# Kernel optimization log

Hardware: AMD Instinct MI355X
Metric: run time of the kernel (lower is better)

Reference implementation:

```python
import jax, jax.numpy as jnp
import numpy as np

B, N, F_IN, F_HID, OUT_DIM = 16, 64, 128, 256, 768
C_IN = 2                      # adjs channels after cat([A, 1-A])
H_T = max(C_IN, OUT_DIM) * 2  # 1536, translate_mlp hidden
D_T = C_IN + 2 * OUT_DIM      # 1538, translate_mlp input
D_R = C_IN + OUT_DIM          # 770, final_read_score input
H_R = 2 * D_R                 # 1540, final_read_score hidden
BN_EPS = 1e-5


def mask_x(x, flags):
    # x: [B,N,F], flags: [B,N]
    return x * flags[:, :, None]


def mask_adjs(adjs, flags):
    # adjs: [B,C,N,N]
    return adjs * (flags[:, None, :, None] * flags[:, None, None, :])


def batchnorm_train(h, gamma, beta):
    # BatchNorm1d in training mode over flattened batch dim (biased var)
    mu = jnp.mean(h, axis=0)
    var = jnp.mean(jnp.square(h - mu), axis=0)
    return gamma * (h - mu) * jax.lax.rsqrt(var + BN_EPS) + beta


def setup_inputs() -> dict:
    key = jax.random.key(0)
    ks = jax.random.split(key, 12)
    def w(k, shape, fan_in):
        return jax.random.normal(k, shape, jnp.float32) / np.float32(np.sqrt(fan_in))
    return {
        "x": jax.random.normal(ks[0], (B, N, F_IN), jnp.float32),
        "adjs": jax.random.uniform(ks[1], (B, N, N), dtype=jnp.float32),
        "node_flags": jnp.ones((B, N), jnp.float32),
        # GIN: multi-channel graph conv (2 channels) + output projection
        "Wg": w(ks[2], (C_IN * F_IN, F_HID), C_IN * F_IN),
        "bg": jnp.zeros((F_HID,), jnp.float32),
        "Wout": w(ks[3], (F_IN + F_HID, OUT_DIM), F_IN + F_HID),
        "bout": jnp.zeros((OUT_DIM,), jnp.float32),
        # translate_mlp: 2-layer MLP with BN, elu
        "W1t": w(ks[4], (D_T, H_T), D_T),
        "b1t": jnp.zeros((H_T,), jnp.float32),
        "gamma_t": jnp.ones((H_T,), jnp.float32),
        "beta_t": jnp.zeros((H_T,), jnp.float32),
        "W2t": w(ks[5], (H_T, OUT_DIM), H_T),
        "b2t": jnp.zeros((OUT_DIM,), jnp.float32),
        # final_read_score: 2-layer MLP, no BN
        "W1r": w(ks[6], (D_R, H_R), D_R),
        "b1r": jnp.zeros((H_R,), jnp.float32),
        "W2r": w(ks[7], (H_R, 1), H_R),
        "b2r": jnp.zeros((1,), jnp.float32),
    }


def reference(x, adjs, node_flags, Wg, bg, Wout, bout,
              W1t, b1t, gamma_t, beta_t, W2t, b2t,
              W1r, b1r, W2r, b2r):
    # ---- build 2-channel adjacency [B,2,N,N] and mask ----
    A = jnp.stack([adjs, 1.0 - adjs], axis=1)
    A = mask_adjs(A, node_flags)

    # ---- GIN (2-channel message passing, dropout=identity / eval) ----
    # per-channel aggregation A_c @ x, concat channels -> [B,N,2*F_IN]
    h = jnp.einsum('bcij,bjf->bicf', A, x).reshape(B, N, C_IN * F_IN)
    h = jax.nn.elu(h @ Wg + bg)
    h = mask_x(h, node_flags)
    x_o = jnp.tanh(jnp.concatenate([x, h], axis=-1) @ Wout + bout)
    x_o = mask_x(x_o, node_flags)  # [B,N,768]

    # ---- node_feature_to_matrix: pairwise features [B,N,N,2*768] ----
    xp = jnp.concatenate([
        jnp.broadcast_to(x_o[:, :, None, :], (B, N, N, OUT_DIM)),
        jnp.broadcast_to(x_o[:, None, :, :], (B, N, N, OUT_DIM)),
    ], axis=-1)
    mlp_in = jnp.concatenate([jnp.transpose(A, (0, 2, 3, 1)), xp], axis=-1)  # [B,N,N,1538]

    # ---- translate_mlp per edge (BN training-mode stats over B*N*N) ----
    flat = mlp_in.reshape(-1, D_T)
    hmid = jax.nn.elu(batchnorm_train(flat @ W1t + b1t, gamma_t, beta_t))
    new_adjs = (hmid @ W2t + b2t).reshape(B, N, N, OUT_DIM).transpose(0, 3, 1, 2)
    new_adjs = new_adjs + jnp.swapaxes(new_adjs, -1, -2)  # symmetrize
    new_adjs = mask_adjs(new_adjs, node_flags)            # [B,768,N,N]

    # ---- final_read_score over stacked channels [B,770,N,N] ----
    stacked = jnp.concatenate([A, new_adjs], axis=1)
    r_in = jnp.transpose(stacked, (0, 2, 3, 1))           # [B,N,N,770]
    hr = jax.nn.elu(r_in @ W1r + b1r)
    score = (hr @ W2r + b2r)[..., 0]                      # [B,N,N]

    mask = 1.0 - jnp.eye(N, dtype=score.dtype)            # zero diagonal
    return (score * mask[None], x_o)
```

## Files before the change

kernel.cpp:

```cpp
#include <hip/hip_runtime.h>
#include <cstdint>
#include <cstddef>

#define NQPAD 1664
#define KC 192
#define NPAIR 2016
#define PROW 2048

typedef __bf16 bf16x8 __attribute__((ext_vector_type(8)));
typedef float  f32x4  __attribute__((ext_vector_type(4)));
typedef unsigned short ushort_t;

__device__ __forceinline__ unsigned short f2bf(float f) {
  union { float f; unsigned u; } v; v.f = f;
  unsigned r = v.u + 0x7fffu + ((v.u >> 16) & 1u);
  return (unsigned short)(r >> 16);
}
__device__ __forceinline__ float bf2f(unsigned short h) {
  union { unsigned u; float f; } v; v.u = ((unsigned)h) << 16;
  return v.f;
}
__device__ __forceinline__ float elu_f(float x) {
  return x > 0.f ? x : __expf(x) - 1.f;
}

__device__ __forceinline__ void cp16_lds(const ushort_t* g, ushort_t* l) {
  __builtin_amdgcn_global_load_lds(
      (const __attribute__((address_space(1))) void*)g,
      (__attribute__((address_space(3))) void*)l, 16, 0, 0);
}

__global__ void k_zero(float* p, int n) {
  int i = blockIdx.x * blockDim.x + threadIdx.x;
  if (i < n) p[i] = 0.f;
}

__global__ void k_diag(float* out) {
  int t = blockIdx.x * 256 + threadIdx.x;
  int b = t >> 6, i = t & 63;
  out[((size_t)b * 64 + i) * 64 + i] = 0.f;
}

__global__ void k_agg(const float* __restrict__ x, const float* __restrict__ adjs,
                      const float* __restrict__ flags,
                      float* __restrict__ h0, float* __restrict__ concat) {
  const int bi = blockIdx.x;
  const int b = bi >> 6, i = bi & 63;
  const int f = threadIdx.x;
  __shared__ float sa[64], sm[64];
  if (f < 64) {
    float m = flags[b * 64 + i] * flags[b * 64 + f];
    float a = adjs[(size_t)(b * 64 + i) * 64 + f] * m;
    sa[f] = a; sm[f] = m;
  }
  __syncthreads();
  float s0 = 0.f, s1 = 0.f;
  const float* xb = x + (size_t)b * 64 * 128;
  for (int j = 0; j < 64; ++j) {
    float xv = xb[j * 128 + f];
    s0 = fmaf(sa[j], xv, s0);
    s1 = fmaf(sm[j] - sa[j], xv, s1);
  }
  h0[(size_t)bi * 256 + f]       = s0;
  h0[(size_t)bi * 256 + 128 + f] = s1;
  concat[(size_t)bi * 384 + f]   = xb[i * 128 + f];
}

__global__ __launch_bounds__(256) void k_sgemm(
    const float* __restrict__ A, const float* __restrict__ Bm,
    float* __restrict__ Cf, ushort_t* __restrict__ Cb,
    const float* __restrict__ bias, const float* __restrict__ rowscale,
    int K, int lda, int ldb, int ldc, int act) {
  __shared__ float As[64 * 17];
  __shared__ float Bs[16 * 64];
  const int tid = threadIdx.x;
  const int tx = tid & 15, ty = tid >> 4;
  const int m0 = blockIdx.y * 64, n0 = blockIdx.x * 64;
  float acc[4][4] = {};
  for (int k0 = 0; k0 < K; k0 += 16) {
#pragma unroll
    for (int i = 0; i < 4; i++) {
      int e = tid + i * 256;
      int r = e >> 4, c = e & 15;
      As[r * 17 + c] = A[(size_t)(m0 + r) * lda + k0 + c];
      int rb = e >> 6, cb = e & 63;
      Bs[e] = Bm[(size_t)(k0 + rb) * ldb + n0 + cb];
    }
    __syncthreads();
#pragma unroll
    for (int kk = 0; kk < 16; kk++) {
      float av[4], bv[4];
#pragma unroll
      for (int i = 0; i < 4; i++) av[i] = As[(ty * 4 + i) * 17 + kk];
#pragma unroll
      for (int j = 0; j < 4; j++) bv[j] = Bs[kk * 64 + tx * 4 + j];
#pragma unroll
      for (int i = 0; i < 4; i++)
#pragma unroll
        for (int j = 0; j < 4; j++) acc[i][j] = fmaf(av[i], bv[j], acc[i][j]);
    }
    __syncthreads();
  }
#pragma unroll
  for (int i = 0; i < 4; i++) {
    const int mm = m0 + ty * 4 + i;
    const float rs = rowscale ? rowscale[mm] : 1.f;
#pragma unroll
    for (int j = 0; j < 4; j++) {
      const int nn = n0 + tx * 4 + j;
      float v = acc[i][j] + (bias ? bias[nn] : 0.f);
      if (act == 1) v = elu_f(v);
      else if (act == 2) v = tanhf(v);
      v *= rs;
      if (Cf) Cf[(size_t)mm * ldc + nn] = v;
      if (Cb) Cb[(size_t)mm * ldc + nn] = f2bf(v);
    }
  }
}

__global__ void k_castT(const float* __restrict__ in, ushort_t* __restrict__ out,
                        int R, int C, int Cpad, int r0, int ld) {
  __shared__ float t[32][33];
  const int rb = blockIdx.y * 32, cb = blockIdx.x * 32;
  const int tx = threadIdx.x, ty = threadIdx.y;
#pragma unroll
  for (int dy = 0; dy < 32; dy += 8) {
    int r = rb + ty + dy, c = cb + tx;
    t[ty + dy][tx] = (r < R && c < C) ? in[(size_t)(r0 + r) * ld + c] : 0.f;
  }
  __syncthreads();
#pragma unroll
  for (int dy = 0; dy < 32; dy += 8) {
    int c = cb + ty + dy, r = rb + tx;
    if (c < Cpad && r < R) out[(size_t)c * R + r] = f2bf(t[tx][ty + dy]);
  }
}

__global__ void k_cast(const float* __restrict__ in, ushort_t* __restrict__ out, int n) {
  int i = blockIdx.x * blockDim.x + threadIdx.x;
  if (i < n) out[i] = f2bf(in[i]);
}

__global__ __launch_bounds__(256) void k_gemm(
    const ushort_t* __restrict__ A, const ushort_t* __restrict__ BT,
    float* __restrict__ outF, ushort_t* __restrict__ outB,
    int K, int lda, int ldb, int ldc, int ncap, int tiledB) {
  __shared__ __align__(16) ushort_t As[128 * 32];
  __shared__ __align__(16) ushort_t Bs[128 * 32];
  const int tid = threadIdx.x;
  const int lane = tid & 63;
  const int wv = tid >> 6;
  const int m0 = blockIdx.y * 128;
  const int n0 = blockIdx.x * 128;
  const int wm = wv >> 1, wn = wv & 1;

  f32x4 z4 = {0.f, 0.f, 0.f, 0.f};
  f32x4 acc[4][4];
#pragma unroll
  for (int i = 0; i < 4; i++)
#pragma unroll
    for (int j = 0; j < 4; j++) acc[i][j] = z4;

  const int srow = lane & 15;
  const int schunk = lane >> 4;
  const ushort_t* gA0 = A + (size_t)(m0 + 2 * wv * 16 + srow) * lda + schunk * 8;
  const ushort_t* gA1 = gA0 + (size_t)16 * lda;
  const ushort_t* gB0 = BT + (size_t)(n0 + 2 * wv * 16 + srow) * ldb + schunk * 8;
  const ushort_t* gB1 = gB0 + (size_t)16 * ldb;
  ushort_t* lA0 = &As[(2 * wv) * 512];
  ushort_t* lA1 = &As[(2 * wv + 1) * 512];
  ushort_t* lB0 = &Bs[(2 * wv) * 512];
  ushort_t* lB1 = &Bs[(2 * wv + 1) * 512];

  for (int k0 = 0; k0 < K; k0 += 32) {
    cp16_lds(gA0 + k0, lA0);
    cp16_lds(gA1 + k0, lA1);
    cp16_lds(gB0 + k0, lB0);
    cp16_lds(gB1 + k0, lB1);
    __syncthreads();
    bf16x8 af[4], bfv[4];
#pragma unroll
    for (int f = 0; f < 4; ++f) {
      af[f]  = *reinterpret_cast<const bf16x8*>(&As[(wm * 4 + f) * 512 + lane * 8]);
      bfv[f] = *reinterpret_cast<const bf16x8*>(&Bs[(wn * 4 + f) * 512 + lane * 8]);
    }
#pragma unroll
    for (int fm = 0; fm < 4; ++fm)
#pragma unroll
      for (int fn = 0; fn < 4; ++fn)
        acc[fm][fn] = __builtin_amdgcn_mfma_f32_16x16x32_bf16(af[fm], bfv[fn], acc[fm][fn], 0, 0, 0);
    __syncthreads();
  }

  const int er = (lane >> 4) * 4;
  const int ec = lane & 15;
#pragma unroll
  for (int fm = 0; fm < 4; ++fm) {
#pragma unroll
    for (int fn = 0; fn < 4; ++fn) {
      const int nn = n0 + wn * 64 + fn * 16 + ec;
      if (nn >= ncap) continue;
#pragma unroll
      for (int r = 0; r < 4; ++r) {
        const int mm = m0 + wm * 64 + fm * 16 + er + r;
        float v = acc[fm][fn][r];
        if (outF) outF[(size_t)mm * ldc + nn] = v;
        if (outB) {
          if (tiledB)
            outB[((size_t)(mm >> 4) * KC + (nn >> 3)) * 128 + (mm & 15) * 8 + (nn & 7)] = f2bf(v);
          else
            outB[(size_t)mm * ldc + nn] = f2bf(v);
        }
      }
    }
  }
}

__global__ __launch_bounds__(256) void k_gemm_t(
    const ushort_t* __restrict__ At, const ushort_t* __restrict__ Bt,
    ushort_t* __restrict__ outB, int ldc, int ncap, int swz) {
  __shared__ __align__(16) ushort_t As[128 * 32];
  __shared__ __align__(16) ushort_t Bs[128 * 32];
  const int tid = threadIdx.x;
  const int lane = tid & 63;
  const int wv = tid >> 6;

  int bx = blockIdx.x, by = blockIdx.y;
  if (swz && (gridDim.y & 7) == 0) {
    int nb = gridDim.x;
    int linear = bx + nb * by;
    int xcd = linear & 7;
    int slot = linear >> 3;
    int mper = gridDim.y >> 3;
    int mp = slot / nb;
    int n  = slot - mp * nb;
    bx = n; by = xcd * mper + mp;
  }
  const int m0 = by * 128;
  const int n0 = bx * 128;
  const int wm = wv >> 1, wn = wv & 1;

  f32x4 z4 = {0.f, 0.f, 0.f, 0.f};
  f32x4 acc[4][4];
#pragma unroll
  for (int i = 0; i < 4; i++)
#pragma unroll
    for (int j = 0; j < 4; j++) acc[i][j] = z4;

  const ushort_t* gA0 = At + ((size_t)(by * 8 + 2 * wv) * KC) * 128 + lane * 8;
  const ushort_t* gA1 = gA0 + (size_t)KC * 128;
  const ushort_t* gB0 = Bt + ((size_t)(bx * 8 + 2 * wv) * KC) * 128 + lane * 8;
  const ushort_t* gB1 = gB0 + (size_t)KC * 128;
  ushort_t* lA0 = &As[(2 * wv) * 512];
  ushort_t* lA1 = &As[(2 * wv + 1) * 512];
  ushort_t* lB0 = &Bs[(2 * wv) * 512];
  ushort_t* lB1 = &Bs[(2 * wv + 1) * 512];

  for (int c0 = 0; c0 < KC; c0 += 4) {
    const size_t go = (size_t)c0 * 128;
    cp16_lds(gA0 + go, lA0);
    cp16_lds(gA1 + go, lA1);
    cp16_lds(gB0 + go, lB0);
    cp16_lds(gB1 + go, lB1);
    __syncthreads();
    bf16x8 af[4], bfv[4];
#pragma unroll
    for (int f = 0; f < 4; ++f) {
      af[f]  = *reinterpret_cast<const bf16x8*>(&As[(wm * 4 + f) * 512 + lane * 8]);
      bfv[f] = *reinterpret_cast<const bf16x8*>(&Bs[(wn * 4 + f) * 512 + lane * 8]);
    }
#pragma unroll
    for (int fm = 0; fm < 4; ++fm)
#pragma unroll
      for (int fn = 0; fn < 4; ++fn)
        acc[fm][fn] = __builtin_amdgcn_mfma_f32_16x16x32_bf16(af[fm], bfv[fn], acc[fm][fn], 0, 0, 0);
    __syncthreads();
  }

  const int er = (lane >> 4) * 4;
  const int ec = lane & 15;
#pragma unroll
  for (int fm = 0; fm < 4; ++fm) {
#pragma unroll
    for (int fn = 0; fn < 4; ++fn) {
      const int nn = n0 + wn * 64 + fn * 16 + ec;
      if (nn >= ncap) continue;
#pragma unroll
      for (int r = 0; r < 4; ++r) {
        const int mm = m0 + wm * 64 + fm * 16 + er + r;
        outB[(size_t)mm * ldc + nn] = f2bf(acc[fm][fn][r]);
      }
    }
  }
}

__global__ void k_pdat(const float* __restrict__ adjs, const float* __restrict__ flags,
                       float4* __restrict__ pdat) {
  const int b = blockIdx.x;
  const int p = blockIdx.y * 256 + threadIdx.x;
  float4 v;
  if (p < NPAIR) {
    int i = (int)((127.f - sqrtf(16129.f - 8.f * (float)p)) * 0.5f);
    if (i < 0) i = 0;
    while (63 * (i + 1) - (((i + 1) * i) >> 1) <= p) ++i;
    while (63 * i - ((i * (i - 1)) >> 1) > p) --i;
    int j = p - (63 * i - ((i * (i - 1)) >> 1)) + i + 1;
    float m = flags[b * 64 + i] * flags[b * 64 + j];
    float a0ij = adjs[((size_t)b * 64 + i) * 64 + j] * m;
    float a0ji = adjs[((size_t)b * 64 + j) * 64 + i] * m;
    v = make_float4(a0ij, a0ji, m, __int_as_float(i * 64 + j));
  } else {
    v = make_float4(0.f, 0.f, 0.f, __int_as_float(-1));
  }
  pdat[(size_t)b * PROW + p] = v;
}

__global__ __launch_bounds__(256) void k_score2(
    const ushort_t* __restrict__ q, const float4* __restrict__ pdat,
    const float* __restrict__ W1r, const float* __restrict__ b1r,
    const float* __restrict__ W2r, const float* __restrict__ dvec2,
    const float* __restrict__ b2r, float* __restrict__ out, int b0) {
  const int p = blockIdx.x;
  const int bl = blockIdx.y;
  const int b = b0 + bl;
  const int t = threadIdx.x;
  float4 pd = pdat[(size_t)b * PROW + p];
  const int ij = __float_as_int(pd.w);
  const int i = ij >> 6, j = ij & 63;
  const float m = pd.z;
  const float a0ij = pd.x, a1ij = m - pd.x;
  const float a0ji = pd.y, a1ji = m - pd.y;
  const ushort_t* qp = q + ((size_t)bl * PROW + p) * NQPAD;
  float s1 = 0.f, s2 = 0.f;
  for (int n = t; n < 1540; n += 256) {
    float quv = bf2f(qp[n]) + dvec2[n];
    float base = fmaf(m, quv, b1r[n]);
    float w0 = W1r[n], w1 = W1r[1540 + n], w2 = W2r[n];
    float z1 = base + a0ij * w0 + a1ij * w1;
    float z2 = base + a0ji * w0 + a1ji * w1;
    s1 = fmaf(elu_f(z1), w2, s1);
    s2 = fmaf(elu_f(z2), w2, s2);
  }
  __shared__ float red[512];
  red[t] = s1; red[256 + t] = s2;
  __syncthreads();
  for (int s = 128; s > 0; s >>= 1) {
    if (t < s) { red[t] += red[t + s]; red[256 + t] += red[256 + t + s]; }
    __syncthreads();
  }
  if (t == 0) {
    out[((size_t)b * 64 + i) * 64 + j] = red[0]   + b2r[0];
    out[((size_t)b * 64 + j) * 64 + i] = red[256] + b2r[0];
  }
}

__global__ void k_dvec(const float* __restrict__ b2t, const float* __restrict__ W1r,
                       float* __restrict__ dvec2) {
  int n = blockIdx.x * 256 + threadIdx.x;
  if (n >= 1540) return;
  int m0 = blockIdx.y * 96;
  float s = 0.f;
  for (int m2 = m0; m2 < m0 + 96; ++m2)
    s = fmaf(b2t[m2], W1r[(size_t)(2 + m2) * 1540 + n], s);
  atomicAdd(&dvec2[n], 2.f * s);
}

__global__ __launch_bounds__(64) void k_adjsum(
    const float* __restrict__ adjs, const float* __restrict__ flags,
    float* __restrict__ r0s, float* __restrict__ r1s,
    float* __restrict__ c0s, float* __restrict__ c1s, float* __restrict__ scal) {
  const int b = blockIdx.x, t = threadIdx.x;
  __shared__ float f[64];
  __shared__ float red[192];
  f[t] = flags[b * 64 + t];
  __syncthreads();
  const float ft = f[t];
  float r0 = 0, r1 = 0, q0 = 0, q1 = 0, pp = 0;
  for (int j = 0; j < 64; ++j) {
    float m = ft * f[j];
    float a = adjs[((size_t)b * 64 + t) * 64 + j] * m;
    float a1 = m - a;
    r0 += a; r1 += a1;
    q0 = fmaf(a, a, q0); q1 = fmaf(a1, a1, q1); pp = fmaf(a, a1, pp);
  }
  r0s[b * 64 + t] = r0; r1s[b * 64 + t] = r1;
  float c0 = 0, c1 = 0;
  for (int i = 0; i < 64; ++i) {
    float m = f[i] * ft;
    float a = adjs[((size_t)b * 64 + i) * 64 + t] * m;
    c0 += a; c1 += m - a;
  }
  c0s[b * 64 + t] = c0; c1s[b * 64 + t] = c1;
  red[t] = r0; red[64 + t] = r1; red[128 + t] = q0;
  __syncthreads();
  for (int s = 32; s > 0; s >>= 1) {
    if (t < s) { red[t] += red[t + s]; red[64 + t] += red[64 + t + s]; red[128 + t] += red[128 + t + s]; }
    __syncthreads();
  }
  if (t == 0) { scal[b * 5 + 0] = red[0]; scal[b * 5 + 1] = red[64]; scal[b * 5 + 2] = red[128]; }
  __syncthreads();
  red[t] = q1; red[64 + t] = pp;
  __syncthreads();
  for (int s = 32; s > 0; s >>= 1) {
    if (t < s) { red[t] += red[t + s]; red[64 + t] += red[64 + t + s]; }
    __syncthreads();
  }
  if (t == 0) { scal[b * 5 + 3] = red[0]; scal[b * 5 + 4] = red[64]; }
}

__global__ __launch_bounds__(256) void k_stats2(
    const float* __restrict__ UV, const float* __restrict__ W1t,
    const float* __restrict__ b1t,
    const float* __restrict__ r0s, const float* __restrict__ r1s,
    const float* __restrict__ c0s, const float* __restrict__ c1s,
    const float* __restrict__ scal,
    float* __restrict__ colsum, float* __restrict__ colss) {
  const int b = blockIdx.x;
  const int n = blockIdx.y * 256 + threadIdx.x;
  const int t = threadIdx.x;
  __shared__ float sr0[64], sr1[64], sc0[64], sc1[64];
  if (t < 64) {
    sr0[t] = r0s[b * 64 + t]; sr1[t] = r1s[b * 64 + t];
    sc0[t] = c0s[b * 64 + t]; sc1[t] = c1s[b * 64 + t];
  }
  __syncthreads();
  const float S0 = scal[b * 5], S1 = scal[b * 5 + 1], Q0 = scal[b * 5 + 2],
              Q1 = scal[b * 5 + 3], P = scal[b * 5 + 4];
  const float w0 = W1t[n], w1 = W1t[1536 + n], beta = b1t[n];
  float eU = 0, eV = 0, qU = 0, qV = 0, ur0 = 0, ur1 = 0, vc0 = 0, vc1 = 0;
  const float* base = UV + (size_t)b * 64 * 3072;
  for (int idx = 0; idx < 64; ++idx) {
    float U = base[(size_t)idx * 3072 + n];
    float V = base[(size_t)idx * 3072 + 1536 + n];
    eU += U; eV += V;
    qU = fmaf(U, U, qU); qV = fmaf(V, V, qV);
    ur0 = fmaf(U, sr0[idx], ur0); ur1 = fmaf(U, sr1[idx], ur1);
    vc0 = fmaf(V, sc0[idx], vc0); vc1 = fmaf(V, sc1[idx], vc1);
  }
  float hsum = 64.f * (eU + eV) + S0 * w0 + S1 * w1 + 4096.f * beta;
  float hss = 64.f * (qU + qV) + Q0 * w0 * w0 + Q1 * w1 * w1 + 4096.f * beta * beta
    + 2.f * (eU * eV + w0 * ur0 + w1 * ur1 + w0 * vc0 + w1 * vc1
             + 64.f * beta * (eU + eV) + w0 * w1 * P + beta * (w0 * S0 + w1 * S1));
  atomicAdd(&colsum[n], hsum);
  atomicAdd(&colss[n], hss);
}

__global__ void k_bnfin(const float* __restrict__ colsum, const float* __restrict__ colss,
                        const float* __restrict__ gamma, const float* __restrict__ beta,
                        float* __restrict__ bns, float* __restrict__ bnt) {
  int n = blockIdx.x * 256 + threadIdx.x;
  if (n >= 1536) return;
  float mu = colsum[n] * (1.f / 65536.f);
  float var = colss[n] * (1.f / 65536.f) - mu * mu;
  float s = gamma[n] * rsqrtf(var + 1e-5f);
  bns[n] = s;
  bnt[n] = beta[n] - mu * s;
}

__global__ __launch_bounds__(256) void k_act4(
    const float* __restrict__ UV, const float4* __restrict__ pdat,
    const float* __restrict__ W1t, const float* __restrict__ b1t,
    const float* __restrict__ bns, const float* __restrict__ bnt,
    ushort_t* __restrict__ hmid_s, int b0) {
  const int g = blockIdx.x;
  const int b = b0 + (g >> 7);
  const int p0 = (g & 127) * 16;
  const int t = threadIdx.x;
  __shared__ __align__(16) ushort_t tile[KC * 128];
  float w06[6], w16[6], s6[6], t6[6], bb6[6];
#pragma unroll
  for (int c = 0; c < 6; c++) {
    int n = t + 256 * c;
    w06[c] = W1t[n]; w16[c] = W1t[1536 + n];
    s6[c] = bns[n]; t6[c] = bnt[n]; bb6[c] = b1t[n];
  }
  const unsigned short zbf = 0;
  for (int ei = 0; ei < 16; ++ei) {
    const int p = p0 + ei;
    float4 pd = pdat[(size_t)b * PROW + p];
    int ij = __float_as_int(pd.w);
    if (ij >= 0) {
      int i = ij >> 6, j = ij & 63;
      const float* Ui = UV + (size_t)(b * 64 + i) * 3072;
      const float* Vi = Ui + 1536;
      const float* Uj = UV + (size_t)(b * 64 + j) * 3072;
      const float* Vj = Uj + 1536;
      float m = pd.z;
      float a0ij = pd.x, a1ij = m - pd.x;
      float a0ji = pd.y, a1ji = m - pd.y;
#pragma unroll
      for (int c = 0; c < 6; c++) {
        int n = t + 256 * c;
        float h1 = Ui[n] + Vj[n] + a0ij * w06[c] + a1ij * w16[c] + bb6[c];
        float h2 = Uj[n] + Vi[n] + a0ji * w06[c] + a1ji * w16[c] + bb6[c];
        float v = elu_f(fmaf(h1, s6[c], t6[c])) + elu_f(fmaf(h2, s6[c], t6[c]));
        int cc = n >> 3;
        int s = (ei + cc) & 15;
        tile[cc * 128 + s * 8 + (n & 7)] = f2bf(v);
      }
    } else {
#pragma unroll
      for (int c = 0; c < 6; c++) {
        int n = t + 256 * c;
        int cc = n >> 3;
        int s = (ei + cc) & 15;
        tile[cc * 128 + s * 8 + (n & 7)] = zbf;
      }
    }
  }
  __syncthreads();
  uint4* gout = (uint4*)(hmid_s + (size_t)g * (KC * 128));
  const uint4* lt = (const uint4*)tile;
#pragma unroll
  for (int it = 0; it < 12; ++it) {
    int u = t + 256 * it;
    int cc = u >> 4, r = u & 15;
    gout[u] = lt[cc * 16 + ((r + cc) & 15)];
  }
}

extern "C" void kernel_launch(void* const* d_in, const int* in_sizes, int n_in,
                              void* d_out, int out_size, void* d_ws, size_t ws_size,
                              hipStream_t stream) {
  const float* x     = (const float*)d_in[0];
  const float* adjs  = (const float*)d_in[1];
  const float* flags = (const float*)d_in[2];
  const float* Wg    = (const float*)d_in[3];
  const float* bg    = (const float*)d_in[4];
  const float* Wout  = (const float*)d_in[5];
  const float* bout  = (const float*)d_in[6];
  const float* W1t   = (const float*)d_in[7];
  const float* b1t   = (const float*)d_in[8];
  const float* gamma = (const float*)d_in[9];
  const float* beta  = (const float*)d_in[10];
  const float* W2t   = (const float*)d_in[11];
  const float* b2t   = (const float*)d_in[12];
  const float* W1r   = (const float*)d_in[13];
  const float* b1r   = (const float*)d_in[14];
  const float* W2r   = (const float*)d_in[15];
  const float* b2r   = (const float*)d_in[16];
  float* out_score = (float*)d_out;
  float* out_xo    = (float*)d_out + 65536;

  uint8_t* ws = (uint8_t*)d_ws;
  size_t off = 0;
  auto alloc = [&](size_t bytes) -> void* {
    void* p = ws + off;
    off += (bytes + 255) & ~(size_t)255;
    return p;
  };
  float*    h0      = (float*)   alloc((size_t)1024 * 256 * 4);
  float*    concat  = (float*)   alloc((size_t)1024 * 384 * 4);
  ushort_t* xo_bf   = (ushort_t*)alloc((size_t)1024 * 768 * 2);
  ushort_t* W1tT    = (ushort_t*)alloc((size_t)3072 * 768 * 2);
  ushort_t* W2t_bf  = (ushort_t*)alloc((size_t)1536 * 768 * 2);
  ushort_t* WrxT    = (ushort_t*)alloc((size_t)NQPAD * 768 * 2);
  ushort_t* WcT     = (ushort_t*)alloc((size_t)NQPAD * 1536 * 2);
  float*    UV      = (float*)   alloc((size_t)1024 * 3072 * 4);
  float*    dvec2   = (float*)   alloc((size_t)1664 * 4);
  float*    colsum  = (float*)   alloc((size_t)1536 * 4);
  float*    colss   = (float*)   alloc((size_t)1536 * 4);
  float*    bns     = (float*)   alloc((size_t)1536 * 4);
  float*    bnt     = (float*)   alloc((size_t)1536 * 4);
  float*    r0s     = (float*)   alloc((size_t)1024 * 4);
  float*    r1s     = (float*)   alloc((size_t)1024 * 4);
  float*    c0s     = (float*)   alloc((size_t)1024 * 4);
  float*    c1s     = (float*)   alloc((size_t)1024 * 4);
  float*    scal    = (float*)   alloc((size_t)80 * 4);
  float4*   pdat    = (float4*)  alloc((size_t)16 * PROW * 16);

  int cb = 2;
  {
    const int cands[4] = {16, 8, 4, 2};
    for (int ci = 0; ci < 4; ++ci) {
      int c = cands[ci];
      size_t need = off + ((size_t)c * PROW * 1536 * 2 + 256)
                        + ((size_t)c * PROW * NQPAD * 2 + 256);
      if (need <= ws_size) { cb = c; break; }
    }
  }
  ushort_t* hmid_s  = (ushort_t*)alloc((size_t)cb * PROW * 1536 * 2);
  ushort_t* q_c     = (ushort_t*)alloc((size_t)cb * PROW * NQPAD * 2);
  (void)in_sizes; (void)n_in; (void)out_size;

  k_zero<<<dim3(19), dim3(256), 0, stream>>>(dvec2, 1664 + 1536 + 1536);
  k_diag<<<dim3(4), dim3(256), 0, stream>>>(out_score);

  k_agg<<<dim3(1024), dim3(128), 0, stream>>>(x, adjs, flags, h0, concat);
  k_sgemm<<<dim3(4, 16), dim3(256), 0, stream>>>(h0, Wg, concat + 128, (ushort_t*)nullptr,
                                                 bg, flags, 256, 256, 256, 384, 1);
  k_sgemm<<<dim3(12, 16), dim3(256), 0, stream>>>(concat, Wout, out_xo, xo_bf,
                                                  bout, flags, 384, 384, 768, 768, 2);

  k_castT<<<dim3(48, 24), dim3(32, 8), 0, stream>>>(W1t, W1tT, 768, 1536, 1536, 2, 1536);
  k_castT<<<dim3(48, 24), dim3(32, 8), 0, stream>>>(W1t, W1tT + (size_t)1536 * 768, 768, 1536, 1536, 770, 1536);
  k_castT<<<dim3(52, 24), dim3(32, 8), 0, stream>>>(W1r, WrxT, 768, 1540, NQPAD, 2, 1540);
  k_cast<<<dim3(4608), dim3(256), 0, stream>>>(W2t, W2t_bf, 1536 * 768);
  k_adjsum<<<dim3(16), dim3(64), 0, stream>>>(adjs, flags, r0s, r1s, c0s, c1s, scal);
  k_pdat<<<dim3(16, 8), dim3(256), 0, stream>>>(adjs, flags, pdat);

  k_gemm<<<dim3(24, 8), dim3(256), 0, stream>>>(xo_bf, W1tT, UV, (ushort_t*)nullptr,
                                                768, 768, 768, 3072, 3072, 0);
  k_gemm<<<dim3(12, 13), dim3(256), 0, stream>>>(WrxT, W2t_bf, (float*)nullptr, WcT,
                                                 768, 768, 768, 1536, 1536, 1);
  k_dvec<<<dim3(7, 8), dim3(256), 0, stream>>>(b2t, W1r, dvec2);

  k_stats2<<<dim3(16, 6), dim3(256), 0, stream>>>(UV, W1t, b1t, r0s, r1s, c0s, c1s, scal,
                                                  colsum, colss);
  k_bnfin<<<dim3(6), dim3(256), 0, stream>>>(colsum, colss, gamma, beta, bns, bnt);

  for (int b0 = 0; b0 < 16; b0 += cb) {
    k_act4<<<dim3(cb * 128), dim3(256), 0, stream>>>(UV, pdat, W1t, b1t, bns, bnt,
                                                     hmid_s, b0);
    k_gemm_t<<<dim3(13, cb * 16), dim3(256), 0, stream>>>(hmid_s, WcT, q_c,
                                                          NQPAD, 1540, 1);
    k_score2<<<dim3(NPAIR, cb), dim3(256), 0, stream>>>(q_c, pdat, W1r, b1r, W2r,
                                                        dvec2, b2r, out_score, b0);
  }
}
```

Measured before the change: 538.9 us.

## Merge prep kernels, vectorize score reduction, narrow q stride, restructure act loop

Merges the zero and diagonal-clear kernels into one launch, and the three transposed casts plus the W2t cast into one 3D-grid launch, cutting launch count. Narrows the q buffer row stride from 1664 to 1544 to shrink the intermediate's memory traffic. k_score2 now reads 8 bf16 values per thread in one vector load and reduces with wave shuffles instead of a shared-memory tree. k_act4 swaps its loop order so each column's weights are loaded once and the row-i U/V values are reused across consecutive pairs with the same i. The q stride must stay consistent with what the GEMM writes; a 1544-element row is 16-byte aligned, so the uint4 load should be valid.

```diff
diff --git a/kernel.cpp b/kernel.cpp
--- a/kernel.cpp
+++ b/kernel.cpp
@@ -3,6 +3,7 @@
 #include <cstddef>
 
 #define NQPAD 1664
+#define QLD 1544
 #define KC 192
 #define NPAIR 2016
 #define PROW 2048
@@ -30,15 +31,13 @@
       (__attribute__((address_space(3))) void*)l, 16, 0, 0);
 }
 
-__global__ void k_zero(float* p, int n) {
-  int i = blockIdx.x * blockDim.x + threadIdx.x;
-  if (i < n) p[i] = 0.f;
-}
-
-__global__ void k_diag(float* out) {
-  int t = blockIdx.x * 256 + threadIdx.x;
-  int b = t >> 6, i = t & 63;
-  out[((size_t)b * 64 + i) * 64 + i] = 0.f;
+__global__ void k_prep(float* acc, int nacc, float* out) {
+  int id = blockIdx.x * 256 + threadIdx.x;
+  if (id < nacc) acc[id] = 0.f;
+  if (id < 1024) {
+    int b = id >> 6, i = id & 63;
+    out[((size_t)b * 64 + i) * 64 + i] = 0.f;
+  }
 }
 
 __global__ void k_agg(const float* __restrict__ x, const float* __restrict__ adjs,
@@ -118,10 +117,11 @@
   }
 }
 
-__global__ void k_castT(const float* __restrict__ in, ushort_t* __restrict__ out,
-                        int R, int C, int Cpad, int r0, int ld) {
+__device__ __forceinline__ void castT_body(const float* in, ushort_t* out,
+                                           int R, int C, int Cpad, int r0, int ld,
+                                           int bx, int by) {
   __shared__ float t[32][33];
-  const int rb = blockIdx.y * 32, cb = blockIdx.x * 32;
+  const int rb = by * 32, cb = bx * 32;
   const int tx = threadIdx.x, ty = threadIdx.y;
 #pragma unroll
   for (int dy = 0; dy < 32; dy += 8) {
@@ -136,9 +136,22 @@
   }
 }
 
-__global__ void k_cast(const float* __restrict__ in, ushort_t* __restrict__ out, int n) {
-  int i = blockIdx.x * blockDim.x + threadIdx.x;
-  if (i < n) out[i] = f2bf(in[i]);
+__global__ void k_wprep(const float* __restrict__ W1t, const float* __restrict__ W1r,
+                        const float* __restrict__ W2t,
+                        ushort_t* __restrict__ W1tT, ushort_t* __restrict__ WrxT,
+                        ushort_t* __restrict__ W2t_bf) {
+  const int z = blockIdx.z;
+  if (z == 0) {
+    if (blockIdx.x < 48) castT_body(W1t, W1tT, 768, 1536, 1536, 2, 1536, blockIdx.x, blockIdx.y);
+  } else if (z == 1) {
+    if (blockIdx.x < 48) castT_body(W1t, W1tT + (size_t)1536 * 768, 768, 1536, 1536, 770, 1536, blockIdx.x, blockIdx.y);
+  } else if (z == 2) {
+    castT_body(W1r, WrxT, 768, 1540, NQPAD, 2, 1540, blockIdx.x, blockIdx.y);
+  } else {
+    int id = (blockIdx.y * 52 + blockIdx.x) * 256 + threadIdx.y * 32 + threadIdx.x;
+    for (int e = id; e < 1536 * 768; e += 52 * 24 * 256)
+      W2t_bf[e] = f2bf(W2t[e]);
+  }
 }
 
 __global__ __launch_bounds__(256) void k_gemm(
@@ -330,27 +343,36 @@
   const float m = pd.z;
   const float a0ij = pd.x, a1ij = m - pd.x;
   const float a0ji = pd.y, a1ji = m - pd.y;
-  const ushort_t* qp = q + ((size_t)bl * PROW + p) * NQPAD;
   float s1 = 0.f, s2 = 0.f;
-  for (int n = t; n < 1540; n += 256) {
-    float quv = bf2f(qp[n]) + dvec2[n];
-    float base = fmaf(m, quv, b1r[n]);
-    float w0 = W1r[n], w1 = W1r[1540 + n], w2 = W2r[n];
-    float z1 = base + a0ij * w0 + a1ij * w1;
-    float z2 = base + a0ji * w0 + a1ji * w1;
-    s1 = fmaf(elu_f(z1), w2, s1);
-    s2 = fmaf(elu_f(z2), w2, s2);
-  }
-  __shared__ float red[512];
-  red[t] = s1; red[256 + t] = s2;
-  __syncthreads();
-  for (int s = 128; s > 0; s >>= 1) {
-    if (t < s) { red[t] += red[t + s]; red[256 + t] += red[256 + t + s]; }
-    __syncthreads();
-  }
+  const int n0 = t * 8;
+  if (n0 < 1540) {
+    const ushort_t* qp = q + ((size_t)bl * PROW + p) * QLD + n0;
+    uint4 qv = *(const uint4*)qp;
+#pragma unroll
+    for (int k = 0; k < 8; ++k) {
+      int n = n0 + k;
+      if (n < 1540) {
+        float quv = bf2f(((const ushort_t*)&qv)[k]) + dvec2[n];
+        float base = fmaf(m, quv, b1r[n]);
+        float w0 = W1r[n], w1 = W1r[1540 + n], w2 = W2r[n];
+        float z1 = base + a0ij * w0 + a1ij * w1;
+        float z2 = base + a0ji * w0 + a1ji * w1;
+        s1 = fmaf(elu_f(z1), w2, s1);
+        s2 = fmaf(elu_f(z2), w2, s2);
+      }
+    }
+  }
+#pragma unroll
+  for (int mask = 1; mask < 64; mask <<= 1) {
+    s1 += __shfl_xor(s1, mask, 64);
+    s2 += __shfl_xor(s2, mask, 64);
+  }
+  __shared__ float r1[4], r2[4];
+  if ((t & 63) == 0) { r1[t >> 6] = s1; r2[t >> 6] = s2; }
+  __syncthreads();
   if (t == 0) {
-    out[((size_t)b * 64 + i) * 64 + j] = red[0]   + b2r[0];
-    out[((size_t)b * 64 + j) * 64 + i] = red[256] + b2r[0];
+    out[((size_t)b * 64 + i) * 64 + j] = r1[0] + r1[1] + r1[2] + r1[3] + b2r[0];
+    out[((size_t)b * 64 + j) * 64 + i] = r2[0] + r2[1] + r2[2] + r2[3] + b2r[0];
   }
 }
 
@@ -467,44 +489,39 @@
   const int p0 = (g & 127) * 16;
   const int t = threadIdx.x;
   __shared__ __align__(16) ushort_t tile[KC * 128];
-  float w06[6], w16[6], s6[6], t6[6], bb6[6];
-#pragma unroll
-  for (int c = 0; c < 6; c++) {
-    int n = t + 256 * c;
-    w06[c] = W1t[n]; w16[c] = W1t[1536 + n];
-    s6[c] = bns[n]; t6[c] = bnt[n]; bb6[c] = b1t[n];
-  }
-  const unsigned short zbf = 0;
-  for (int ei = 0; ei < 16; ++ei) {
-    const int p = p0 + ei;
-    float4 pd = pdat[(size_t)b * PROW + p];
-    int ij = __float_as_int(pd.w);
-    if (ij >= 0) {
-      int i = ij >> 6, j = ij & 63;
-      const float* Ui = UV + (size_t)(b * 64 + i) * 3072;
-      const float* Vi = Ui + 1536;
-      const float* Uj = UV + (size_t)(b * 64 + j) * 3072;
-      const float* Vj = Uj + 1536;
-      float m = pd.z;
-      float a0ij = pd.x, a1ij = m - pd.x;
-      float a0ji = pd.y, a1ji = m - pd.y;
-#pragma unroll
-      for (int c = 0; c < 6; c++) {
-        int n = t + 256 * c;
-        float h1 = Ui[n] + Vj[n] + a0ij * w06[c] + a1ij * w16[c] + bb6[c];
-        float h2 = Uj[n] + Vi[n] + a0ji * w06[c] + a1ji * w16[c] + bb6[c];
-        float v = elu_f(fmaf(h1, s6[c], t6[c])) + elu_f(fmaf(h2, s6[c], t6[c]));
-        int cc = n >> 3;
-        int s = (ei + cc) & 15;
-        tile[cc * 128 + s * 8 + (n & 7)] = f2bf(v);
-      }
-    } else {
-#pragma unroll
-      for (int c = 0; c < 6; c++) {
-        int n = t + 256 * c;
-        int cc = n >> 3;
-        int s = (ei + cc) & 15;
-        tile[cc * 128 + s * 8 + (n & 7)] = zbf;
+  __shared__ float4 spd[16];
+  if (t < 16) spd[t] = pdat[(size_t)b * PROW + p0 + t];
+  __syncthreads();
+  const float* base = UV + (size_t)b * 64 * 3072;
+  for (int c = 0; c < 6; ++c) {
+    const int n = t + 256 * c;
+    const float w0 = W1t[n], w1 = W1t[1536 + n];
+    const float ss = bns[n], tt = bnt[n];
+    const float bb = b1t[n];
+    const int cc = n >> 3;
+    const int lo = n & 7;
+    int ilast = -1;
+    float ui = 0.f, vi = 0.f;
+    for (int ei = 0; ei < 16; ++ei) {
+      float4 pd = spd[ei];
+      int ij = __float_as_int(pd.w);
+      int s = (ei + cc) & 15;
+      if (ij >= 0) {
+        int i = ij >> 6, j = ij & 63;
+        if (i != ilast) {
+          ui = base[(size_t)i * 3072 + n];
+          vi = base[(size_t)i * 3072 + 1536 + n];
+          ilast = i;
+        }
+        float uj = base[(size_t)j * 3072 + n];
+        float vj = base[(size_t)j * 3072 + 1536 + n];
+        float m = pd.z;
+        float h1 = ui + vj + pd.x * w0 + (m - pd.x) * w1 + bb;
+        float h2 = uj + vi + pd.y * w0 + (m - pd.y) * w1 + bb;
+        float v = elu_f(fmaf(h1, ss, tt)) + elu_f(fmaf(h2, ss, tt));
+        tile[cc * 128 + s * 8 + lo] = f2bf(v);
+      } else {
+        tile[cc * 128 + s * 8 + lo] = 0;
       }
     }
   }
@@ -575,16 +592,15 @@
     for (int ci = 0; ci < 4; ++ci) {
       int c = cands[ci];
       size_t need = off + ((size_t)c * PROW * 1536 * 2 + 256)
-                        + ((size_t)c * PROW * NQPAD * 2 + 256);
+                        + ((size_t)c * PROW * QLD * 2 + 256);
       if (need <= ws_size) { cb = c; break; }
     }
   }
   ushort_t* hmid_s  = (ushort_t*)alloc((size_t)cb * PROW * 1536 * 2);
-  ushort_t* q_c     = (ushort_t*)alloc((size_t)cb * PROW * NQPAD * 2);
+  ushort_t* q_c     = (ushort_t*)alloc((size_t)cb * PROW * QLD * 2);
   (void)in_sizes; (void)n_in; (void)out_size;
 
-  k_zero<<<dim3(19), dim3(256), 0, stream>>>(dvec2, 1664 + 1536 + 1536);
-  k_diag<<<dim3(4), dim3(256), 0, stream>>>(out_score);
+  k_prep<<<dim3(19), dim3(256), 0, stream>>>(dvec2, 1664 + 1536 + 1536, out_score);
 
   k_agg<<<dim3(1024), dim3(128), 0, stream>>>(x, adjs, flags, h0, concat);
   k_sgemm<<<dim3(4, 16), dim3(256), 0, stream>>>(h0, Wg, concat + 128, (ushort_t*)nullptr,
@@ -592,10 +608,7 @@
   k_sgemm<<<dim3(12, 16), dim3(256), 0, stream>>>(concat, Wout, out_xo, xo_bf,
                                                   bout, flags, 384, 384, 768, 768, 2);
 
-  k_castT<<<dim3(48, 24), dim3(32, 8), 0, stream>>>(W1t, W1tT, 768, 1536, 1536, 2, 1536);
-  k_castT<<<dim3(48, 24), dim3(32, 8), 0, stream>>>(W1t, W1tT + (size_t)1536 * 768, 768, 1536, 1536, 770, 1536);
-  k_castT<<<dim3(52, 24), dim3(32, 8), 0, stream>>>(W1r, WrxT, 768, 1540, NQPAD, 2, 1540);
-  k_cast<<<dim3(4608), dim3(256), 0, stream>>>(W2t, W2t_bf, 1536 * 768);
+  k_wprep<<<dim3(52, 24, 4), dim3(32, 8), 0, stream>>>(W1t, W1r, W2t, W1tT, WrxT, W2t_bf);
   k_adjsum<<<dim3(16), dim3(64), 0, stream>>>(adjs, flags, r0s, r1s, c0s, c1s, scal);
   k_pdat<<<dim3(16, 8), dim3(256), 0, stream>>>(adjs, flags, pdat);
 
@@ -613,7 +626,7 @@
     k_act4<<<dim3(cb * 128), dim3(256), 0, stream>>>(UV, pdat, W1t, b1t, bns, bnt,
                                                      hmid_s, b0);
     k_gemm_t<<<dim3(13, cb * 16), dim3(256), 0, stream>>>(hmid_s, WcT, q_c,
-                                                          NQPAD, 1540, 1);
+                                                          QLD, 1540, 1);
     k_score2<<<dim3(NPAIR, cb), dim3(256), 0, stream>>>(q_c, pdat, W1r, b1r, W2r,
                                                         dvec2, b2r, out_score, b0);
   }
```

After: 780.1 us. 1.45x slower.
